# Optimization experiments

Hardware: AMD Instinct MI355X
Metric: run time of the kernel (lower is better)

The kernel has to match this reference:

```python
import jax, jax.numpy as jnp
import numpy as np

B, S, D = 1, 2048, 2048          # batch, context_length, embedding_dimension
H, DH = 16, 128                  # num_heads, head_size (= head_output_dimension)
HID = 4 * D                      # SwiGLU hidden dim
LAMBDA_INIT = 0.8
EPS = 1e-6


def setup_inputs() -> dict:
    key = jax.random.key(0)
    ks = jax.random.split(key, 14)
    nrm = lambda k, sh, s=0.02: jax.random.normal(k, sh, jnp.float32) * s
    return {
        "x": jax.random.normal(ks[0], (B, S, D), jnp.float32),
        "g_norm": jnp.ones((D,), jnp.float32),          # shared RMSNorm gain (same layer used twice)
        "Wq1": nrm(ks[1], (H, D, DH)), "Wq2": nrm(ks[2], (H, D, DH)),
        "Wk1": nrm(ks[3], (H, D, DH)), "Wk2": nrm(ks[4], (H, D, DH)),
        "Wv":  nrm(ks[5], (H, D, DH)),
        "lq1": nrm(ks[6], (H, DH), 0.1), "lk1": nrm(ks[7], (H, DH), 0.1),
        "lq2": nrm(ks[8], (H, DH), 0.1), "lk2": nrm(ks[9], (H, DH), 0.1),
        "Wo": nrm(ks[10], (H * DH, D)),
        "W1": nrm(ks[11], (D, HID)), "W2": nrm(ks[12], (D, HID)), "W3": nrm(ks[13], (HID, D)),
    }


def rmsnorm(x, g):
    return x * jax.lax.rsqrt(jnp.mean(x * x, axis=-1, keepdims=True) + EPS) * g


def diff_attention(x, Wq1, Wq2, Wk1, Wk2, Wv, lq1, lk1, lq2, lk2, Wo):
    # per-head projections: [B,S,D] x [H,D,DH] -> [B,H,S,DH]
    proj = lambda W: jnp.einsum('bsd,hde->bhse', x, W)
    q1, q2 = proj(Wq1), proj(Wq2)
    k1, k2 = proj(Wk1), proj(Wk2)
    v = proj(Wv)
    scale = 1.0 / jnp.sqrt(jnp.float32(DH))
    A1 = jax.nn.softmax(jnp.einsum('bhse,bhte->bhst', q1, k1) * scale, axis=-1)
    A2 = jax.nn.softmax(jnp.einsum('bhse,bhte->bhst', q2, k2) * scale, axis=-1)
    # learned per-head lambda: exp(lq1.lk1) - exp(lq2.lk2) + lambda_init
    lam = (jnp.exp(jnp.sum(lq1 * lk1, -1)) - jnp.exp(jnp.sum(lq2 * lk2, -1)) + LAMBDA_INIT)  # [H]
    o = jnp.einsum('bhst,bhte->bhse', A1 - lam[None, :, None, None] * A2, v)  # [B,H,S,DH]
    o = o.transpose(0, 2, 1, 3).reshape(B, S, H * DH)
    return o @ Wo


def reference(x, g_norm, Wq1, Wq2, Wk1, Wk2, Wv, lq1, lk1, lq2, lk2, Wo, W1, W2, W3):
    # Encoder block (dropout=0 -> identity in eval)
    h = rmsnorm(x, g_norm)
    h = diff_attention(h, Wq1, Wq2, Wk1, Wk2, Wv, lq1, lk1, lq2, lk2, Wo) + h
    z = rmsnorm(h, g_norm)
    ffn = (jax.nn.silu(z @ W1) * (z @ W2)) @ W3  # SwiGLU
    return ffn + h
```

## Files before the change

### kernel.cpp

```cpp
#include <hip/hip_runtime.h>

typedef unsigned short u16;
typedef __bf16 bf16x8 __attribute__((ext_vector_type(8)));
typedef float f32x4 __attribute__((ext_vector_type(4)));

#define S_LEN 2048
#define D_DIM 2048
#define NH 16
#define DH 128
#define HID 8192

__device__ __forceinline__ u16 f2bf(float f) {
  unsigned int u = __float_as_uint(f);
  u += 0x7fff + ((u >> 16) & 1);
  return (u16)(u >> 16);
}

__device__ __forceinline__ void gld16(const u16* g, u16* l) {
  __builtin_amdgcn_global_load_lds(
      (const __attribute__((address_space(1))) unsigned int*)g,
      (__attribute__((address_space(3))) unsigned int*)l, 16, 0, 0);
}

__global__ __launch_bounds__(256) void tconv_f2b(const float* __restrict__ in,
                                                 u16* __restrict__ out, int R, int C) {
  __shared__ float tile[32][33];
  size_t boff = (size_t)blockIdx.z * R * C;
  in += boff; out += boff;
  int c0 = blockIdx.x * 32, r0 = blockIdx.y * 32;
  int tx = threadIdx.x, ty = threadIdx.y;
#pragma unroll
  for (int i = 0; i < 32; i += 8) tile[ty + i][tx] = in[(size_t)(r0 + ty + i) * C + c0 + tx];
  __syncthreads();
#pragma unroll
  for (int i = 0; i < 32; i += 8) out[(size_t)(c0 + ty + i) * R + r0 + tx] = f2bf(tile[tx][ty + i]);
}

__global__ __launch_bounds__(256) void tconv_b2b(const u16* __restrict__ in,
                                                 u16* __restrict__ out, int R, int C) {
  __shared__ u16 tile[32][34];
  size_t boff = (size_t)blockIdx.z * R * C;
  in += boff; out += boff;
  int c0 = blockIdx.x * 32, r0 = blockIdx.y * 32;
  int tx = threadIdx.x, ty = threadIdx.y;
#pragma unroll
  for (int i = 0; i < 32; i += 8) tile[ty + i][tx] = in[(size_t)(r0 + ty + i) * C + c0 + tx];
  __syncthreads();
#pragma unroll
  for (int i = 0; i < 32; i += 8) out[(size_t)(c0 + ty + i) * R + r0 + tx] = tile[tx][ty + i];
}

__global__ __launch_bounds__(256) void rmsnorm_kernel(const float* __restrict__ x,
                                                      const float* __restrict__ g,
                                                      float* __restrict__ xf,
                                                      u16* __restrict__ xb) {
  int row = blockIdx.x;
  int t = threadIdx.x;
  const float4* xr = (const float4*)(x + (size_t)row * D_DIM);
  float4 v0 = xr[t];
  float4 v1 = xr[t + 256];
  float ss = v0.x * v0.x + v0.y * v0.y + v0.z * v0.z + v0.w * v0.w +
             v1.x * v1.x + v1.y * v1.y + v1.z * v1.z + v1.w * v1.w;
#pragma unroll
  for (int o = 1; o < 64; o <<= 1) ss += __shfl_xor(ss, o, 64);
  __shared__ float wss[4];
  if ((t & 63) == 0) wss[t >> 6] = ss;
  __syncthreads();
  float tot = wss[0] + wss[1] + wss[2] + wss[3];
  float rs = rsqrtf(tot * (1.0f / D_DIM) + 1e-6f);
  const float4* gr = (const float4*)g;
  float4 g0 = gr[t], g1 = gr[t + 256];
  float4 o0, o1;
  o0.x = v0.x * rs * g0.x; o0.y = v0.y * rs * g0.y; o0.z = v0.z * rs * g0.z; o0.w = v0.w * rs * g0.w;
  o1.x = v1.x * rs * g1.x; o1.y = v1.y * rs * g1.y; o1.z = v1.z * rs * g1.z; o1.w = v1.w * rs * g1.w;
  if (xf) {
    float4* xfr = (float4*)(xf + (size_t)row * D_DIM);
    xfr[t] = o0; xfr[t + 256] = o1;
  }
  ushort4 b0, b1;
  b0.x = f2bf(o0.x); b0.y = f2bf(o0.y); b0.z = f2bf(o0.z); b0.w = f2bf(o0.w);
  b1.x = f2bf(o1.x); b1.y = f2bf(o1.y); b1.z = f2bf(o1.z); b1.w = f2bf(o1.w);
  ushort4* xbr = (ushort4*)(xb + (size_t)row * D_DIM);
  xbr[t] = b0; xbr[t + 256] = b1;
}

__global__ __launch_bounds__(256) void lam_kernel(const float* __restrict__ lq1,
                                                  const float* __restrict__ lk1,
                                                  const float* __restrict__ lq2,
                                                  const float* __restrict__ lk2,
                                                  float* __restrict__ lamw) {
  int t = threadIdx.x;
  int h = t >> 4, i = (t & 15) << 3;
  float d1 = 0.f, d2 = 0.f;
#pragma unroll
  for (int j = 0; j < 8; j++) {
    d1 += lq1[h * DH + i + j] * lk1[h * DH + i + j];
    d2 += lq2[h * DH + i + j] * lk2[h * DH + i + j];
  }
#pragma unroll
  for (int o = 1; o < 16; o <<= 1) { d1 += __shfl_xor(d1, o, 64); d2 += __shfl_xor(d2, o, 64); }
  if ((t & 15) == 0) lamw[h] = __expf(d1) - __expf(d2) + 0.8f;
}

__global__ __launch_bounds__(512) void gemm8_proj(const u16* __restrict__ A,
                                                  const u16* __restrict__ Bt,
                                                  u16* __restrict__ Out,
                                                  int M, int N, int K) {
  constexpr int BM = 256, BN = 128, BK = 64, NBUF = 3;
  __shared__ __align__(16) u16 As[NBUF][BM * BK];
  __shared__ __align__(16) u16 Bs[NBUF][BN * BK];
  const int t = threadIdx.x;
  const int lane = t & 63;
  const int wid = t >> 6;
  const int wm = (wid >> 2) * 128;
  const int wn = (wid & 3) * 32;
  const int fr = lane & 15, fq = lane >> 4;
  const int m0 = blockIdx.y * BM, n0 = blockIdx.x * BN;

  f32x4 acc[8][2] = {};

  const int sro = t >> 3;
  const int scol = ((((t & 7) ^ (sro & 7)) << 4) >> 1);
  const u16* aSrc = A + (size_t)(m0 + sro) * K + scol;
  const u16* bSrc = Bt + (size_t)(n0 + sro) * K + scol;

  const int NT = K >> 6;

#define STAGE_A(buf, k0, s) gld16(aSrc + (size_t)((s)*64) * K + (k0), &As[buf][(s)*4096 + t * 8])
#define STAGE_B(buf, k0, s) gld16(bSrc + (size_t)((s)*64) * K + (k0), &Bs[buf][(s)*4096 + t * 8])

  STAGE_A(0, 0, 0); STAGE_A(0, 0, 1); STAGE_A(0, 0, 2); STAGE_A(0, 0, 3);
  STAGE_B(0, 0, 0); STAGE_B(0, 0, 1);
  STAGE_A(1, BK, 0); STAGE_A(1, BK, 1); STAGE_A(1, BK, 2); STAGE_A(1, BK, 3);
  STAGE_B(1, BK, 0); STAGE_B(1, BK, 1);
  asm volatile("s_waitcnt vmcnt(6)" ::: "memory");
  __builtin_amdgcn_s_barrier();

  const int swz = (fr & 7) << 4;

  for (int tk = 0; tk < NT; ++tk) {
    const int r = tk % 3;
    const int pf = tk + 2;
    const int pbuf = pf % 3;
    const bool doPf = pf < NT;
    const int k0pf = pf << 6;

    bf16x8 bfrag[2][2];
#pragma unroll
    for (int j = 0; j < 2; ++j)
#pragma unroll
      for (int kk = 0; kk < 2; ++kk) {
        int row = wn + j * 16 + fr;
        int cb = (kk * 64 + fq * 16) ^ swz;
        bfrag[j][kk] = *(const bf16x8*)&Bs[r][row * 64 + (cb >> 1)];
      }

#pragma unroll
    for (int ph = 0; ph < 2; ++ph) {
      if (doPf) {
        if (ph == 0) { STAGE_A(pbuf, k0pf, 0); STAGE_A(pbuf, k0pf, 1); STAGE_B(pbuf, k0pf, 0); }
        else         { STAGE_A(pbuf, k0pf, 2); STAGE_A(pbuf, k0pf, 3); STAGE_B(pbuf, k0pf, 1); }
      }
      bf16x8 af[4][2];
#pragma unroll
      for (int i = 0; i < 4; ++i)
#pragma unroll
        for (int kk = 0; kk < 2; ++kk) {
          int row = wm + ph * 64 + i * 16 + fr;
          int cb = (kk * 64 + fq * 16) ^ swz;
          af[i][kk] = *(const bf16x8*)&As[r][row * 64 + (cb >> 1)];
        }
      __builtin_amdgcn_s_setprio(1);
#pragma unroll
      for (int i = 0; i < 4; ++i)
#pragma unroll
        for (int j = 0; j < 2; ++j) {
          acc[ph * 4 + i][j] =
              __builtin_amdgcn_mfma_f32_16x16x32_bf16(af[i][0], bfrag[j][0], acc[ph * 4 + i][j], 0, 0, 0);
          acc[ph * 4 + i][j] =
              __builtin_amdgcn_mfma_f32_16x16x32_bf16(af[i][1], bfrag[j][1], acc[ph * 4 + i][j], 0, 0, 0);
        }
      __builtin_amdgcn_s_setprio(0);
    }

    if (tk + 1 < NT) {
      if (doPf) asm volatile("s_waitcnt vmcnt(6)" ::: "memory");
      else      asm volatile("s_waitcnt vmcnt(0)" ::: "memory");
      __builtin_amdgcn_s_barrier();
    }
  }

#undef STAGE_A
#undef STAGE_B

  const size_t headBase = (size_t)(n0 >> 7) * ((size_t)S_LEN * 128);
#pragma unroll
  for (int i = 0; i < 8; ++i)
#pragma unroll
    for (int j = 0; j < 2; ++j) {
      int row0 = m0 + wm + i * 16 + (fq << 2);
      int colL = wn + j * 16 + fr;
#pragma unroll
      for (int rr = 0; rr < 4; ++rr)
        Out[headBase + (size_t)(row0 + rr) * 128 + colL] = f2bf(acc[i][j][rr]);
    }
}

template <int MODE, int BN>
__global__ __launch_bounds__(256) void gemm_a(const u16* __restrict__ A,
                                              const u16* __restrict__ Bt,
                                              const u16* __restrict__ Bt2,
                                              void* __restrict__ Cout,
                                              const float* __restrict__ res,
                                              int M, int N, int K, long sBt, long sC) {
  constexpr int BM = 128, BK = 32;
  constexpr int JF = BN / 32;
  __shared__ __align__(16) u16 As[2][BM * BK];
  __shared__ __align__(16) u16 Bs[2][BN * BK];
  __shared__ __align__(16) u16 Bs2[(MODE == 2) ? 2 : 1][(MODE == 2) ? BN * BK : 8];
  const int t = threadIdx.x;
  const int lane = t & 63, wid = t >> 6;
  const int wm = (wid >> 1) * 64, wn = (wid & 1) * (BN / 2);
  const int fr = lane & 15, fq = lane >> 4;
  const int m0 = blockIdx.y * BM, n0 = blockIdx.x * BN;
  const int bz = blockIdx.z;
  const u16* bt = Bt + (long)bz * sBt;
  f32x4 acc[4][JF] = {};
  f32x4 acc2[(MODE == 2) ? 4 : 1][(MODE == 2) ? JF : 1] = {};
  const int sr = t >> 2, sc = (t & 3) << 3;
  const u16* aG = A + (long)(m0 + sr) * K + sc;
  const u16* bG = bt + (long)(n0 + sr) * K + sc;
  const u16* b2G = (MODE == 2) ? (Bt2 + (long)(n0 + sr) * K + sc) : nullptr;

  auto stage = [&](int buf, int k0) {
    gld16(aG + k0, &As[buf][t * 8]);
    gld16(aG + (long)64 * K + k0, &As[buf][t * 8 + 64 * BK]);
    gld16(bG + k0, &Bs[buf][t * 8]);
    if (BN == 128) gld16(bG + (long)64 * K + k0, &Bs[buf][t * 8 + 64 * BK]);
    if (MODE == 2) {
      gld16(b2G + k0, &Bs2[buf][t * 8]);
      if (BN == 128) gld16(b2G + (long)64 * K + k0, &Bs2[buf][t * 8 + 64 * BK]);
    }
  };

  stage(0, 0);
  __syncthreads();

  int cur = 0;
  for (int k0 = 0; k0 < K; k0 += BK) {
    if (k0 + BK < K) stage(cur ^ 1, k0 + BK);

    bf16x8 af[4], bfr[JF];
#pragma unroll
    for (int i = 0; i < 4; i++) af[i] = *(const bf16x8*)&As[cur][(wm + i * 16 + fr) * BK + fq * 8];
#pragma unroll
    for (int j = 0; j < JF; j++) bfr[j] = *(const bf16x8*)&Bs[cur][(wn + j * 16 + fr) * BK + fq * 8];
    bf16x8 cf[(MODE == 2) ? JF : 1];
    if (MODE == 2) {
#pragma unroll
      for (int j = 0; j < JF; j++) cf[j] = *(const bf16x8*)&Bs2[cur][(wn + j * 16 + fr) * BK + fq * 8];
    }

    __builtin_amdgcn_s_setprio(1);
#pragma unroll
    for (int i = 0; i < 4; i++)
#pragma unroll
      for (int j = 0; j < JF; j++)
        acc[i][j] = __builtin_amdgcn_mfma_f32_16x16x32_bf16(af[i], bfr[j], acc[i][j], 0, 0, 0);
    if (MODE == 2) {
#pragma unroll
      for (int i = 0; i < 4; i++)
#pragma unroll
        for (int j = 0; j < JF; j++)
          acc2[i][j] = __builtin_amdgcn_mfma_f32_16x16x32_bf16(af[i], cf[j], acc2[i][j], 0, 0, 0);
    }
    __builtin_amdgcn_s_setprio(0);

    __syncthreads();
    cur ^= 1;
  }

#pragma unroll
  for (int i = 0; i < 4; i++)
#pragma unroll
    for (int j = 0; j < JF; j++) {
      int row0 = m0 + wm + i * 16 + (fq << 2);
      int col = n0 + wn + j * 16 + fr;
#pragma unroll
      for (int r = 0; r < 4; r++) {
        long idx = (long)(row0 + r) * N + col;
        float v = acc[i][j][r];
        if (MODE == 0) {
          ((u16*)Cout + (long)bz * sC)[idx] = f2bf(v);
        } else if (MODE == 1) {
          ((float*)Cout)[idx] = v + res[idx];
        } else {
          float g2 = acc2[i][j][r];
          float sg = v / (1.0f + __expf(-v));
          ((u16*)Cout)[idx] = f2bf(sg * g2);
        }
      }
    }
}

#define LDK 136
#define LDV 40
#define LDP 40

__global__ __launch_bounds__(256) void flash_attn(const u16* __restrict__ q1g,
                                                  const u16* __restrict__ q2g,
                                                  const u16* __restrict__ k1g,
                                                  const u16* __restrict__ k2g,
                                                  const u16* __restrict__ vtg,
                                                  const float* __restrict__ lamw,
                                                  u16* __restrict__ og) {
  __shared__ __align__(16) u16 Ks1[32 * LDK];
  __shared__ __align__(16) u16 Ks2[32 * LDK];
  __shared__ __align__(16) u16 Vs[128 * LDV];
  __shared__ __align__(16) u16 Ps[4 * 2 * 16 * LDP];
  const float scale = 0.08838834764831845f;
  int h = blockIdx.y, qt = blockIdx.x;
  size_t hoff = (size_t)h * S_LEN * DH;
  const u16* q1 = q1g + hoff;
  const u16* q2 = q2g + hoff;
  const u16* k1 = k1g + hoff;
  const u16* k2 = k2g + hoff;
  const u16* vt = vtg + hoff;
  int t = threadIdx.x, wid = t >> 6, lane = t & 63;
  int fr = lane & 15, fq = lane >> 4;
  int qrow = qt * 64 + wid * 16 + fr;
  bf16x8 qf1[4], qf2[4];
#pragma unroll
  for (int ks = 0; ks < 4; ks++) {
    qf1[ks] = *(const bf16x8*)&q1[(size_t)qrow * DH + ks * 32 + fq * 8];
    qf2[ks] = *(const bf16x8*)&q2[(size_t)qrow * DH + ks * 32 + fq * 8];
  }
  bf16x8 ones;
#pragma unroll
  for (int i = 0; i < 8; i++) ones[i] = (__bf16)1.0f;

  f32x4 O1[8] = {};
  f32x4 O2[8] = {};
  f32x4 L1 = {};
  f32x4 L2 = {};
  int skr = t >> 3, skc = (t & 7) << 4;
  int svr = t >> 2, svc = (t & 3) << 3;
  u16* myP1 = &Ps[(wid * 2 + 0) * 16 * LDP];
  u16* myP2 = &Ps[(wid * 2 + 1) * 16 * LDP];

  for (int kt = 0; kt < S_LEN; kt += 32) {
    uint4 ka1 = *(const uint4*)&k1[(size_t)(kt + skr) * DH + skc];
    uint4 kb1 = *(const uint4*)&k1[(size_t)(kt + skr) * DH + skc + 8];
    uint4 ka2 = *(const uint4*)&k2[(size_t)(kt + skr) * DH + skc];
    uint4 kb2 = *(const uint4*)&k2[(size_t)(kt + skr) * DH + skc + 8];
    uint4 va = *(const uint4*)&vt[(size_t)svr * S_LEN + kt + svc];
    uint4 vb = *(const uint4*)&vt[(size_t)(svr + 64) * S_LEN + kt + svc];
    __syncthreads();
    *(uint4*)&Ks1[skr * LDK + skc] = ka1;
    *(uint4*)&Ks1[skr * LDK + skc + 8] = kb1;
    *(uint4*)&Ks2[skr * LDK + skc] = ka2;
    *(uint4*)&Ks2[skr * LDK + skc + 8] = kb2;
    *(uint4*)&Vs[svr * LDV + svc] = va;
    *(uint4*)&Vs[(svr + 64) * LDV + svc] = vb;
    __syncthreads();

    f32x4 s1[2] = {};
    f32x4 s2[2] = {};
#pragma unroll
    for (int nf = 0; nf < 2; nf++)
#pragma unroll
      for (int ks = 0; ks < 4; ks++) {
        bf16x8 b1v = *(const bf16x8*)&Ks1[(nf * 16 + fr) * LDK + ks * 32 + fq * 8];
        s1[nf] = __builtin_amdgcn_mfma_f32_16x16x32_bf16(qf1[ks], b1v, s1[nf], 0, 0, 0);
        bf16x8 b2v = *(const bf16x8*)&Ks2[(nf * 16 + fr) * LDK + ks * 32 + fq * 8];
        s2[nf] = __builtin_amdgcn_mfma_f32_16x16x32_bf16(qf2[ks], b2v, s2[nf], 0, 0, 0);
      }

#pragma unroll
    for (int nf = 0; nf < 2; nf++)
#pragma unroll
      for (int r = 0; r < 4; r++) {
        myP1[(fq * 4 + r) * LDP + nf * 16 + fr] = f2bf(__expf(s1[nf][r] * scale));
        myP2[(fq * 4 + r) * LDP + nf * 16 + fr] = f2bf(__expf(s2[nf][r] * scale));
      }
    asm volatile("s_waitcnt lgkmcnt(0)" ::: "memory");
    bf16x8 pa1 = *(const bf16x8*)&myP1[fr * LDP + fq * 8];
    bf16x8 pa2 = *(const bf16x8*)&myP2[fr * LDP + fq * 8];
    L1 = __builtin_amdgcn_mfma_f32_16x16x32_bf16(pa1, ones, L1, 0, 0, 0);
    L2 = __builtin_amdgcn_mfma_f32_16x16x32_bf16(pa2, ones, L2, 0, 0, 0);
#pragma unroll
    for (int f = 0; f < 8; f++) {
      bf16x8 bv = *(const bf16x8*)&Vs[(f * 16 + fr) * LDV + fq * 8];
      O1[f] = __builtin_amdgcn_mfma_f32_16x16x32_bf16(pa1, bv, O1[f], 0, 0, 0);
      O2[f] = __builtin_amdgcn_mfma_f32_16x16x32_bf16(pa2, bv, O2[f], 0, 0, 0);
    }
  }

  float lam = lamw[h];
#pragma unroll
  for (int r = 0; r < 4; r++) {
    float i1 = 1.0f / L1[r], i2 = lam / L2[r];
#pragma unroll
    for (int f = 0; f < 8; f++) {
      float val = O1[f][r] * i1 - O2[f][r] * i2;
      og[(size_t)(qt * 64 + wid * 16 + fq * 4 + r) * (NH * DH) + h * DH + f * 16 + fr] =
          f2bf(val);
    }
  }
}

extern "C" void kernel_launch(void* const* d_in, const int* in_sizes, int n_in,
                              void* d_out, int out_size, void* d_ws, size_t ws_size,
                              hipStream_t stream) {
  const float* x = (const float*)d_in[0];
  const float* g = (const float*)d_in[1];
  const float* Wq1 = (const float*)d_in[2];
  const float* Wq2 = (const float*)d_in[3];
  const float* Wk1 = (const float*)d_in[4];
  const float* Wk2 = (const float*)d_in[5];
  const float* Wv = (const float*)d_in[6];
  const float* lq1 = (const float*)d_in[7];
  const float* lk1 = (const float*)d_in[8];
  const float* lq2 = (const float*)d_in[9];
  const float* lk2 = (const float*)d_in[10];
  const float* Wo = (const float*)d_in[11];
  const float* W1 = (const float*)d_in[12];
  const float* W2 = (const float*)d_in[13];
  const float* W3 = (const float*)d_in[14];

  char* ws = (char*)d_ws;
  size_t off = 0;
  auto alloc = [&](size_t b) {
    char* p = ws + off;
    off += (b + 255) & ~(size_t)255;
    return p;
  };
  const size_t PROJ_B = (size_t)NH * DH * D_DIM * 2;
  u16* wq1t = (u16*)alloc(PROJ_B);
  u16* wq2t = (u16*)alloc(PROJ_B);
  u16* wk1t = (u16*)alloc(PROJ_B);
  u16* wk2t = (u16*)alloc(PROJ_B);
  u16* wvt = (u16*)alloc(PROJ_B);
  u16* wot = (u16*)alloc((size_t)D_DIM * NH * DH * 2);
  u16* w1t = (u16*)alloc((size_t)HID * D_DIM * 2);
  u16* w2t = (u16*)alloc((size_t)HID * D_DIM * 2);
  u16* w3t = (u16*)alloc((size_t)D_DIM * HID * 2);
  u16* xnb = (u16*)alloc((size_t)S_LEN * D_DIM * 2);
  float* xnf = (float*)alloc((size_t)S_LEN * D_DIM * 4);
  u16* q1b = (u16*)alloc(PROJ_B);
  u16* q2b = (u16*)alloc(PROJ_B);
  u16* k1b = (u16*)alloc(PROJ_B);
  u16* k2b = (u16*)alloc(PROJ_B);
  u16* vb = (u16*)alloc(PROJ_B);
  u16* vtb = (u16*)alloc(PROJ_B);
  float* lamw = (float*)alloc(NH * 4);
  u16* oa = (u16*)alloc((size_t)S_LEN * NH * DH * 2);
  float* hf = (float*)alloc((size_t)S_LEN * D_DIM * 4);
  u16* zb = (u16*)alloc((size_t)S_LEN * D_DIM * 2);
  u16* ffb = (u16*)alloc((size_t)S_LEN * HID * 2);
  if (off > ws_size) return;

  dim3 tpb(32, 8);
  tconv_f2b<<<dim3(DH / 32, D_DIM / 32, NH), tpb, 0, stream>>>(Wq1, wq1t, D_DIM, DH);
  tconv_f2b<<<dim3(DH / 32, D_DIM / 32, NH), tpb, 0, stream>>>(Wq2, wq2t, D_DIM, DH);
  tconv_f2b<<<dim3(DH / 32, D_DIM / 32, NH), tpb, 0, stream>>>(Wk1, wk1t, D_DIM, DH);
  tconv_f2b<<<dim3(DH / 32, D_DIM / 32, NH), tpb, 0, stream>>>(Wk2, wk2t, D_DIM, DH);
  tconv_f2b<<<dim3(DH / 32, D_DIM / 32, NH), tpb, 0, stream>>>(Wv, wvt, D_DIM, DH);
  tconv_f2b<<<dim3(D_DIM / 32, (NH * DH) / 32, 1), tpb, 0, stream>>>(Wo, wot, NH * DH, D_DIM);
  tconv_f2b<<<dim3(HID / 32, D_DIM / 32, 1), tpb, 0, stream>>>(W1, w1t, D_DIM, HID);
  tconv_f2b<<<dim3(HID / 32, D_DIM / 32, 1), tpb, 0, stream>>>(W2, w2t, D_DIM, HID);
  tconv_f2b<<<dim3(D_DIM / 32, HID / 32, 1), tpb, 0, stream>>>(W3, w3t, HID, D_DIM);

  rmsnorm_kernel<<<S_LEN, 256, 0, stream>>>(x, g, xnf, xnb);
  lam_kernel<<<1, 256, 0, stream>>>(lq1, lk1, lq2, lk2, lamw);

  gemm8_proj<<<dim3((5 * NH * DH) / 128, S_LEN / 256), 512, 0, stream>>>(
      xnb, wq1t, q1b, S_LEN, 5 * NH * DH, D_DIM);
  tconv_b2b<<<dim3(DH / 32, S_LEN / 32, NH), tpb, 0, stream>>>(vb, vtb, S_LEN, DH);

  flash_attn<<<dim3(S_LEN / 64, NH), 256, 0, stream>>>(q1b, q2b, k1b, k2b, vtb, lamw, oa);

  gemm_a<1, 64><<<dim3(D_DIM / 64, S_LEN / 128, 1), 256, 0, stream>>>(
      oa, wot, nullptr, hf, xnf, S_LEN, D_DIM, NH * DH, 0, 0);
  rmsnorm_kernel<<<S_LEN, 256, 0, stream>>>(hf, g, nullptr, zb);
  gemm_a<2, 64><<<dim3(HID / 64, S_LEN / 128, 1), 256, 0, stream>>>(
      zb, w1t, w2t, ffb, nullptr, S_LEN, HID, D_DIM, 0, 0);
  gemm_a<1, 64><<<dim3(D_DIM / 64, S_LEN / 128, 1), 256, 0, stream>>>(
      ffb, w3t, nullptr, d_out, hf, S_LEN, D_DIM, HID, 0, 0);
}
```

Baseline: 979.0 us.

## Use 8-wave triple-buffered GEMM for SwiGLU up-projection and reschedule projection GEMM

Adds a new 512-thread, triple-buffered, swizzled-LDS GEMM kernel for the fused W1/W2 SwiGLU GEMM. It replaces the 256-thread double-buffered gemm_a MODE 2 path with 128x128 tiles and prefetches split into phases. The QKV projection kernel is restructured to interleave prefetch issue with fragment loads, adding barriers and lgkmcnt waits between phases, and gets launch bounds requesting 2 blocks per CU. The aim is better data reuse and overlap of loads with MFMA in the largest GEMM, at the cost of more barriers and LDS pressure (144KB for gemm8s).

```diff
diff --git a/kernel.cpp b/kernel.cpp
--- a/kernel.cpp
+++ b/kernel.cpp
@@ -102,107 +102,230 @@
   if ((t & 15) == 0) lamw[h] = __expf(d1) - __expf(d2) + 0.8f;
 }
 
-__global__ __launch_bounds__(512) void gemm8_proj(const u16* __restrict__ A,
-                                                  const u16* __restrict__ Bt,
-                                                  u16* __restrict__ Out,
-                                                  int M, int N, int K) {
-  constexpr int BM = 256, BN = 128, BK = 64, NBUF = 3;
-  __shared__ __align__(16) u16 As[NBUF][BM * BK];
-  __shared__ __align__(16) u16 Bs[NBUF][BN * BK];
+__global__ __launch_bounds__(512, 2) void gemm8p(const u16* __restrict__ A,
+                                                 const u16* __restrict__ Bt,
+                                                 u16* __restrict__ Out, int K) {
+  __shared__ __align__(16) u16 As[3][256 * 64];
+  __shared__ __align__(16) u16 Bs[3][128 * 64];
   const int t = threadIdx.x;
-  const int lane = t & 63;
-  const int wid = t >> 6;
-  const int wm = (wid >> 2) * 128;
-  const int wn = (wid & 3) * 32;
+  const int lane = t & 63, wid = t >> 6;
+  const int wm = (wid >> 2) * 128, wn = (wid & 3) * 32;
   const int fr = lane & 15, fq = lane >> 4;
-  const int m0 = blockIdx.y * BM, n0 = blockIdx.x * BN;
+  const int n0 = blockIdx.x * 128, m0 = blockIdx.y * 256;
 
   f32x4 acc[8][2] = {};
 
   const int sro = t >> 3;
-  const int scol = ((((t & 7) ^ (sro & 7)) << 4) >> 1);
+  const int scol = ((t & 7) ^ (sro & 7)) << 3;
   const u16* aSrc = A + (size_t)(m0 + sro) * K + scol;
   const u16* bSrc = Bt + (size_t)(n0 + sro) * K + scol;
-
   const int NT = K >> 6;
-
-#define STAGE_A(buf, k0, s) gld16(aSrc + (size_t)((s)*64) * K + (k0), &As[buf][(s)*4096 + t * 8])
-#define STAGE_B(buf, k0, s) gld16(bSrc + (size_t)((s)*64) * K + (k0), &Bs[buf][(s)*4096 + t * 8])
-
-  STAGE_A(0, 0, 0); STAGE_A(0, 0, 1); STAGE_A(0, 0, 2); STAGE_A(0, 0, 3);
-  STAGE_B(0, 0, 0); STAGE_B(0, 0, 1);
-  STAGE_A(1, BK, 0); STAGE_A(1, BK, 1); STAGE_A(1, BK, 2); STAGE_A(1, BK, 3);
-  STAGE_B(1, BK, 0); STAGE_B(1, BK, 1);
+  const int swz = (fr & 7) << 4;
+
+#define PA(buf, kof, s) gld16(aSrc + (size_t)((s)*64) * K + (kof), &As[buf][(s)*4096 + t * 8])
+#define PB(buf, kof, s) gld16(bSrc + (size_t)((s)*64) * K + (kof), &Bs[buf][(s)*4096 + t * 8])
+
+  PA(0, 0, 0); PA(0, 0, 1); PB(0, 0, 0); PA(0, 0, 2); PA(0, 0, 3); PB(0, 0, 1);
+  PA(1, 64, 0); PA(1, 64, 1); PB(1, 64, 0); PA(1, 64, 2); PA(1, 64, 3); PB(1, 64, 1);
   asm volatile("s_waitcnt vmcnt(6)" ::: "memory");
   __builtin_amdgcn_s_barrier();
 
-  const int swz = (fr & 7) << 4;
-
-  for (int tk = 0; tk < NT; ++tk) {
-    const int r = tk % 3;
-    const int pf = tk + 2;
-    const int pbuf = pf % 3;
-    const bool doPf = pf < NT;
-    const int k0pf = pf << 6;
-
-    bf16x8 bfrag[2][2];
+  for (int k = 0; k < NT; ++k) {
+    const int r = k % 3, pbuf = (k + 2) % 3;
+    const bool pf = (k + 2) < NT;
+    const int kof = (k + 2) << 6;
+
+    bf16x8 bfr[2][2], af[4][2];
 #pragma unroll
     for (int j = 0; j < 2; ++j)
 #pragma unroll
       for (int kk = 0; kk < 2; ++kk) {
         int row = wn + j * 16 + fr;
         int cb = (kk * 64 + fq * 16) ^ swz;
-        bfrag[j][kk] = *(const bf16x8*)&Bs[r][row * 64 + (cb >> 1)];
-      }
-
-#pragma unroll
-    for (int ph = 0; ph < 2; ++ph) {
-      if (doPf) {
-        if (ph == 0) { STAGE_A(pbuf, k0pf, 0); STAGE_A(pbuf, k0pf, 1); STAGE_B(pbuf, k0pf, 0); }
-        else         { STAGE_A(pbuf, k0pf, 2); STAGE_A(pbuf, k0pf, 3); STAGE_B(pbuf, k0pf, 1); }
-      }
-      bf16x8 af[4][2];
-#pragma unroll
-      for (int i = 0; i < 4; ++i)
-#pragma unroll
-        for (int kk = 0; kk < 2; ++kk) {
-          int row = wm + ph * 64 + i * 16 + fr;
-          int cb = (kk * 64 + fq * 16) ^ swz;
-          af[i][kk] = *(const bf16x8*)&As[r][row * 64 + (cb >> 1)];
-        }
-      __builtin_amdgcn_s_setprio(1);
-#pragma unroll
-      for (int i = 0; i < 4; ++i)
-#pragma unroll
-        for (int j = 0; j < 2; ++j) {
-          acc[ph * 4 + i][j] =
-              __builtin_amdgcn_mfma_f32_16x16x32_bf16(af[i][0], bfrag[j][0], acc[ph * 4 + i][j], 0, 0, 0);
-          acc[ph * 4 + i][j] =
-              __builtin_amdgcn_mfma_f32_16x16x32_bf16(af[i][1], bfrag[j][1], acc[ph * 4 + i][j], 0, 0, 0);
-        }
-      __builtin_amdgcn_s_setprio(0);
-    }
-
-    if (tk + 1 < NT) {
-      if (doPf) asm volatile("s_waitcnt vmcnt(6)" ::: "memory");
-      else      asm volatile("s_waitcnt vmcnt(0)" ::: "memory");
+        bfr[j][kk] = *(const bf16x8*)&Bs[r][row * 64 + (cb >> 1)];
+      }
+#pragma unroll
+    for (int i = 0; i < 4; ++i)
+#pragma unroll
+      for (int kk = 0; kk < 2; ++kk) {
+        int row = wm + i * 16 + fr;
+        int cb = (kk * 64 + fq * 16) ^ swz;
+        af[i][kk] = *(const bf16x8*)&As[r][row * 64 + (cb >> 1)];
+      }
+    if (pf) { PA(pbuf, kof, 0); PA(pbuf, kof, 1); PB(pbuf, kof, 0); }
+    __builtin_amdgcn_s_barrier();
+    asm volatile("s_waitcnt lgkmcnt(0)" ::: "memory");
+    __builtin_amdgcn_sched_barrier(0);
+    __builtin_amdgcn_s_setprio(1);
+#pragma unroll
+    for (int i = 0; i < 4; ++i)
+#pragma unroll
+      for (int j = 0; j < 2; ++j) {
+        acc[i][j] = __builtin_amdgcn_mfma_f32_16x16x32_bf16(af[i][0], bfr[j][0], acc[i][j], 0, 0, 0);
+        acc[i][j] = __builtin_amdgcn_mfma_f32_16x16x32_bf16(af[i][1], bfr[j][1], acc[i][j], 0, 0, 0);
+      }
+    __builtin_amdgcn_s_setprio(0);
+    __builtin_amdgcn_s_barrier();
+
+#pragma unroll
+    for (int i = 0; i < 4; ++i)
+#pragma unroll
+      for (int kk = 0; kk < 2; ++kk) {
+        int row = wm + 64 + i * 16 + fr;
+        int cb = (kk * 64 + fq * 16) ^ swz;
+        af[i][kk] = *(const bf16x8*)&As[r][row * 64 + (cb >> 1)];
+      }
+    if (pf) { PA(pbuf, kof, 2); PA(pbuf, kof, 3); PB(pbuf, kof, 1); }
+    __builtin_amdgcn_s_barrier();
+    asm volatile("s_waitcnt lgkmcnt(0)" ::: "memory");
+    __builtin_amdgcn_sched_barrier(0);
+    __builtin_amdgcn_s_setprio(1);
+#pragma unroll
+    for (int i = 0; i < 4; ++i)
+#pragma unroll
+      for (int j = 0; j < 2; ++j) {
+        acc[4 + i][j] = __builtin_amdgcn_mfma_f32_16x16x32_bf16(af[i][0], bfr[j][0], acc[4 + i][j], 0, 0, 0);
+        acc[4 + i][j] = __builtin_amdgcn_mfma_f32_16x16x32_bf16(af[i][1], bfr[j][1], acc[4 + i][j], 0, 0, 0);
+      }
+    __builtin_amdgcn_s_setprio(0);
+
+    if (k + 1 < NT) {
+      if (pf) asm volatile("s_waitcnt vmcnt(6)" ::: "memory");
+      else    asm volatile("s_waitcnt vmcnt(0)" ::: "memory");
       __builtin_amdgcn_s_barrier();
     }
   }
-
-#undef STAGE_A
-#undef STAGE_B
+#undef PA
+#undef PB
 
   const size_t headBase = (size_t)(n0 >> 7) * ((size_t)S_LEN * 128);
 #pragma unroll
-  for (int i = 0; i < 8; ++i)
+  for (int i8 = 0; i8 < 8; ++i8)
+#pragma unroll
+    for (int j = 0; j < 2; ++j) {
+      int row0 = m0 + wm + (i8 >> 2) * 64 + (i8 & 3) * 16 + (fq << 2);
+      int colL = wn + j * 16 + fr;
+#pragma unroll
+      for (int rr = 0; rr < 4; ++rr)
+        Out[headBase + (size_t)(row0 + rr) * 128 + colL] = f2bf(acc[i8][j][rr]);
+    }
+}
+
+__global__ __launch_bounds__(512, 2) void gemm8s(const u16* __restrict__ A,
+                                                 const u16* __restrict__ B1t,
+                                                 const u16* __restrict__ B2t,
+                                                 u16* __restrict__ Out, int N, int K) {
+  __shared__ __align__(16) u16 As[3][128 * 64];
+  __shared__ __align__(16) u16 B1s[3][128 * 64];
+  __shared__ __align__(16) u16 B2s[3][128 * 64];
+  const int t = threadIdx.x;
+  const int lane = t & 63, wid = t >> 6;
+  const int wm = (wid >> 2) * 64, wn = (wid & 3) * 32;
+  const int fr = lane & 15, fq = lane >> 4;
+  const int n0 = blockIdx.x * 128, m0 = blockIdx.y * 128;
+
+  f32x4 acc1[4][2] = {};
+  f32x4 acc2[4][2] = {};
+
+  const int sro = t >> 3;
+  const int scol = ((t & 7) ^ (sro & 7)) << 3;
+  const u16* aSrc = A + (size_t)(m0 + sro) * K + scol;
+  const u16* b1Src = B1t + (size_t)(n0 + sro) * K + scol;
+  const u16* b2Src = B2t + (size_t)(n0 + sro) * K + scol;
+  const int NT = K >> 6;
+  const int swz = (fr & 7) << 4;
+
+#define SA(buf, kof, s) gld16(aSrc + (size_t)((s)*64) * K + (kof), &As[buf][(s)*4096 + t * 8])
+#define SB1(buf, kof, s) gld16(b1Src + (size_t)((s)*64) * K + (kof), &B1s[buf][(s)*4096 + t * 8])
+#define SB2(buf, kof, s) gld16(b2Src + (size_t)((s)*64) * K + (kof), &B2s[buf][(s)*4096 + t * 8])
+
+  SA(0, 0, 0); SA(0, 0, 1); SB1(0, 0, 0); SB1(0, 0, 1); SB2(0, 0, 0); SB2(0, 0, 1);
+  SA(1, 64, 0); SA(1, 64, 1); SB1(1, 64, 0); SB1(1, 64, 1); SB2(1, 64, 0); SB2(1, 64, 1);
+  asm volatile("s_waitcnt vmcnt(6)" ::: "memory");
+  __builtin_amdgcn_s_barrier();
+
+  for (int k = 0; k < NT; ++k) {
+    const int r = k % 3, pbuf = (k + 2) % 3;
+    const bool pf = (k + 2) < NT;
+    const int kof = (k + 2) << 6;
+
+    bf16x8 af[4][2], bfr[2][2];
+#pragma unroll
+    for (int i = 0; i < 4; ++i)
+#pragma unroll
+      for (int kk = 0; kk < 2; ++kk) {
+        int row = wm + i * 16 + fr;
+        int cb = (kk * 64 + fq * 16) ^ swz;
+        af[i][kk] = *(const bf16x8*)&As[r][row * 64 + (cb >> 1)];
+      }
+#pragma unroll
+    for (int j = 0; j < 2; ++j)
+#pragma unroll
+      for (int kk = 0; kk < 2; ++kk) {
+        int row = wn + j * 16 + fr;
+        int cb = (kk * 64 + fq * 16) ^ swz;
+        bfr[j][kk] = *(const bf16x8*)&B1s[r][row * 64 + (cb >> 1)];
+      }
+    if (pf) { SA(pbuf, kof, 0); SA(pbuf, kof, 1); SB1(pbuf, kof, 0); }
+    __builtin_amdgcn_s_barrier();
+    asm volatile("s_waitcnt lgkmcnt(0)" ::: "memory");
+    __builtin_amdgcn_sched_barrier(0);
+    __builtin_amdgcn_s_setprio(1);
+#pragma unroll
+    for (int i = 0; i < 4; ++i)
+#pragma unroll
+      for (int j = 0; j < 2; ++j) {
+        acc1[i][j] = __builtin_amdgcn_mfma_f32_16x16x32_bf16(af[i][0], bfr[j][0], acc1[i][j], 0, 0, 0);
+        acc1[i][j] = __builtin_amdgcn_mfma_f32_16x16x32_bf16(af[i][1], bfr[j][1], acc1[i][j], 0, 0, 0);
+      }
+    __builtin_amdgcn_s_setprio(0);
+    __builtin_amdgcn_s_barrier();
+
+#pragma unroll
+    for (int j = 0; j < 2; ++j)
+#pragma unroll
+      for (int kk = 0; kk < 2; ++kk) {
+        int row = wn + j * 16 + fr;
+        int cb = (kk * 64 + fq * 16) ^ swz;
+        bfr[j][kk] = *(const bf16x8*)&B2s[r][row * 64 + (cb >> 1)];
+      }
+    if (pf) { SB1(pbuf, kof, 1); SB2(pbuf, kof, 0); SB2(pbuf, kof, 1); }
+    __builtin_amdgcn_s_barrier();
+    asm volatile("s_waitcnt lgkmcnt(0)" ::: "memory");
+    __builtin_amdgcn_sched_barrier(0);
+    __builtin_amdgcn_s_setprio(1);
+#pragma unroll
+    for (int i = 0; i < 4; ++i)
+#pragma unroll
+      for (int j = 0; j < 2; ++j) {
+        acc2[i][j] = __builtin_amdgcn_mfma_f32_16x16x32_bf16(af[i][0], bfr[j][0], acc2[i][j], 0, 0, 0);
+        acc2[i][j] = __builtin_amdgcn_mfma_f32_16x16x32_bf16(af[i][1], bfr[j][1], acc2[i][j], 0, 0, 0);
+      }
+    __builtin_amdgcn_s_setprio(0);
+
+    if (k + 1 < NT) {
+      if (pf) asm volatile("s_waitcnt vmcnt(6)" ::: "memory");
+      else    asm volatile("s_waitcnt vmcnt(0)" ::: "memory");
+      __builtin_amdgcn_s_barrier();
+    }
+  }
+#undef SA
+#undef SB1
+#undef SB2
+
+#pragma unroll
+  for (int i = 0; i < 4; ++i)
 #pragma unroll
     for (int j = 0; j < 2; ++j) {
       int row0 = m0 + wm + i * 16 + (fq << 2);
-      int colL = wn + j * 16 + fr;
-#pragma unroll
-      for (int rr = 0; rr < 4; ++rr)
-        Out[headBase + (size_t)(row0 + rr) * 128 + colL] = f2bf(acc[i][j][rr]);
+      int col = n0 + wn + j * 16 + fr;
+#pragma unroll
+      for (int rr = 0; rr < 4; ++rr) {
+        float v = acc1[i][j][rr];
+        float g2 = acc2[i][j][rr];
+        float sg = v / (1.0f + __expf(-v));
+        Out[(size_t)(row0 + rr) * N + col] = f2bf(sg * g2);
+      }
     }
 }
 
@@ -217,7 +340,6 @@
   constexpr int JF = BN / 32;
   __shared__ __align__(16) u16 As[2][BM * BK];
   __shared__ __align__(16) u16 Bs[2][BN * BK];
-  __shared__ __align__(16) u16 Bs2[(MODE == 2) ? 2 : 1][(MODE == 2) ? BN * BK : 8];
   const int t = threadIdx.x;
   const int lane = t & 63, wid = t >> 6;
   const int wm = (wid >> 1) * 64, wn = (wid & 1) * (BN / 2);
@@ -226,21 +348,15 @@
   const int bz = blockIdx.z;
   const u16* bt = Bt + (long)bz * sBt;
   f32x4 acc[4][JF] = {};
-  f32x4 acc2[(MODE == 2) ? 4 : 1][(MODE == 2) ? JF : 1] = {};
   const int sr = t >> 2, sc = (t & 3) << 3;
   const u16* aG = A + (long)(m0 + sr) * K + sc;
   const u16* bG = bt + (long)(n0 + sr) * K + sc;
-  const u16* b2G = (MODE == 2) ? (Bt2 + (long)(n0 + sr) * K + sc) : nullptr;
 
   auto stage = [&](int buf, int k0) {
     gld16(aG + k0, &As[buf][t * 8]);
     gld16(aG + (long)64 * K + k0, &As[buf][t * 8 + 64 * BK]);
     gld16(bG + k0, &Bs[buf][t * 8]);
     if (BN == 128) gld16(bG + (long)64 * K + k0, &Bs[buf][t * 8 + 64 * BK]);
-    if (MODE == 2) {
-      gld16(b2G + k0, &Bs2[buf][t * 8]);
-      if (BN == 128) gld16(b2G + (long)64 * K + k0, &Bs2[buf][t * 8 + 64 * BK]);
-    }
   };
 
   stage(0, 0);
@@ -255,11 +371,6 @@
     for (int i = 0; i < 4; i++) af[i] = *(const bf16x8*)&As[cur][(wm + i * 16 + fr) * BK + fq * 8];
 #pragma unroll
     for (int j = 0; j < JF; j++) bfr[j] = *(const bf16x8*)&Bs[cur][(wn + j * 16 + fr) * BK + fq * 8];
-    bf16x8 cf[(MODE == 2) ? JF : 1];
-    if (MODE == 2) {
-#pragma unroll
-      for (int j = 0; j < JF; j++) cf[j] = *(const bf16x8*)&Bs2[cur][(wn + j * 16 + fr) * BK + fq * 8];
-    }
 
     __builtin_amdgcn_s_setprio(1);
 #pragma unroll
@@ -267,13 +378,6 @@
 #pragma unroll
       for (int j = 0; j < JF; j++)
         acc[i][j] = __builtin_amdgcn_mfma_f32_16x16x32_bf16(af[i], bfr[j], acc[i][j], 0, 0, 0);
-    if (MODE == 2) {
-#pragma unroll
-      for (int i = 0; i < 4; i++)
-#pragma unroll
-        for (int j = 0; j < JF; j++)
-          acc2[i][j] = __builtin_amdgcn_mfma_f32_16x16x32_bf16(af[i], cf[j], acc2[i][j], 0, 0, 0);
-    }
     __builtin_amdgcn_s_setprio(0);
 
     __syncthreads();
@@ -290,14 +394,10 @@
       for (int r = 0; r < 4; r++) {
         long idx = (long)(row0 + r) * N + col;
         float v = acc[i][j][r];
-        if (MODE == 0) {
-          ((u16*)Cout + (long)bz * sC)[idx] = f2bf(v);
-        } else if (MODE == 1) {
+        if (MODE == 1) {
           ((float*)Cout)[idx] = v + res[idx];
         } else {
-          float g2 = acc2[i][j][r];
-          float sg = v / (1.0f + __expf(-v));
-          ((u16*)Cout)[idx] = f2bf(sg * g2);
+          ((u16*)Cout + (long)bz * sC)[idx] = f2bf(v);
         }
       }
     }
@@ -474,8 +574,8 @@
   rmsnorm_kernel<<<S_LEN, 256, 0, stream>>>(x, g, xnf, xnb);
   lam_kernel<<<1, 256, 0, stream>>>(lq1, lk1, lq2, lk2, lamw);
 
-  gemm8_proj<<<dim3((5 * NH * DH) / 128, S_LEN / 256), 512, 0, stream>>>(
-      xnb, wq1t, q1b, S_LEN, 5 * NH * DH, D_DIM);
+  gemm8p<<<dim3((5 * NH * DH) / 128, S_LEN / 256), 512, 0, stream>>>(
+      xnb, wq1t, q1b, D_DIM);
   tconv_b2b<<<dim3(DH / 32, S_LEN / 32, NH), tpb, 0, stream>>>(vb, vtb, S_LEN, DH);
 
   flash_attn<<<dim3(S_LEN / 64, NH), 256, 0, stream>>>(q1b, q2b, k1b, k2b, vtb, lamw, oa);
@@ -483,8 +583,8 @@
   gemm_a<1, 64><<<dim3(D_DIM / 64, S_LEN / 128, 1), 256, 0, stream>>>(
       oa, wot, nullptr, hf, xnf, S_LEN, D_DIM, NH * DH, 0, 0);
   rmsnorm_kernel<<<S_LEN, 256, 0, stream>>>(hf, g, nullptr, zb);
-  gemm_a<2, 64><<<dim3(HID / 64, S_LEN / 128, 1), 256, 0, stream>>>(
-      zb, w1t, w2t, ffb, nullptr, S_LEN, HID, D_DIM, 0, 0);
+  gemm8s<<<dim3(HID / 128, S_LEN / 128), 512, 0, stream>>>(
+      zb, w1t, w2t, ffb, HID, D_DIM);
   gemm_a<1, 64><<<dim3(D_DIM / 64, S_LEN / 128, 1), 256, 0, stream>>>(
       ffb, w3t, nullptr, d_out, hf, S_LEN, D_DIM, HID, 0, 0);
 }
```

New measurement: 946.9 us. 3.3% less time.
